# Performance work log

Measured on AMD Instinct MI355X. Metric: run time of the kernel, lower is better.

## Reference

```python
import jax, jax.numpy as jnp
import numpy as np

N_EMBD = 384
N_HEAD = 6
BLOCK_SIZE = 256


def setup_inputs() -> dict:
    key = jax.random.key(0)
    ks = jax.random.split(key, 5)
    B, T = 128, 256
    x = jax.random.normal(ks[0], (B, T, N_EMBD), dtype=jnp.float32)
    # torch nn.Linear weights are (out_features, in_features)
    w_attn = jax.random.normal(ks[1], (3 * N_EMBD, N_EMBD), dtype=jnp.float32) * (1.0 / np.sqrt(N_EMBD))
    b_attn = jax.random.normal(ks[2], (3 * N_EMBD,), dtype=jnp.float32) * 0.02
    w_proj = jax.random.normal(ks[3], (N_EMBD, N_EMBD), dtype=jnp.float32) * (1.0 / np.sqrt(N_EMBD))
    b_proj = jax.random.normal(ks[4], (N_EMBD,), dtype=jnp.float32) * 0.02
    return {"x": x, "w_attn": w_attn, "b_attn": b_attn, "w_proj": w_proj, "b_proj": b_proj}


def reference(x, w_attn, b_attn, w_proj, b_proj):
    B, T, C = x.shape
    hd = C // N_HEAD  # head dim = 64
    qkv = x @ w_attn.T + b_attn                      # [B,T,3C]
    q, k, v = jnp.split(qkv, 3, axis=2)
    # [B,T,C] -> [B,H,T,hd]
    q = q.reshape(B, T, N_HEAD, hd).transpose(0, 2, 1, 3)
    k = k.reshape(B, T, N_HEAD, hd).transpose(0, 2, 1, 3)
    v = v.reshape(B, T, N_HEAD, hd).transpose(0, 2, 1, 3)
    att = jnp.einsum("bhqd,bhkd->bhqk", q, k) * (1.0 / np.sqrt(hd))
    causal = jnp.tril(jnp.ones((T, T), dtype=bool))
    att = jnp.where(causal, att, -jnp.inf)
    att = jax.nn.softmax(att, axis=-1)
    y = jnp.einsum("bhqk,bhkd->bhqd", att, v)        # [B,H,T,hd]
    y = y.transpose(0, 2, 1, 3).reshape(B, T, C)
    return y @ w_proj.T + b_proj
```

## Files before the change

kernel.cpp:

```cpp
#include <hip/hip_runtime.h>
#include <stdint.h>


typedef unsigned short u16;
typedef __attribute__((ext_vector_type(8))) short short8;
typedef __attribute__((ext_vector_type(4))) short short4v;
typedef __attribute__((ext_vector_type(4))) float float4v;

__device__ __forceinline__ u16 f2b(float f){
  union { float f; uint32_t u; } cv; cv.f = f;
  uint32_t u = cv.u;
  u += 0x7FFFu + ((u >> 16) & 1u);
  return (u16)(u >> 16);
}

__device__ __forceinline__ float4v mfma16(short8 a, short8 b, float4v c){
  return __builtin_amdgcn_mfma_f32_16x16x32_bf16(a, b, c, 0, 0, 0);
}

__device__ __forceinline__ void gld16(const void* g, void* l){
  __builtin_amdgcn_global_load_lds((__attribute__((address_space(1))) const void*)g,
                                   (__attribute__((address_space(3))) void*)l, 16, 0, 0);
}

__global__ __launch_bounds__(256) void cvt3(
    const float* __restrict__ a, u16* __restrict__ da, int na,
    const float* __restrict__ b, u16* __restrict__ db, int nb,
    const float* __restrict__ c, u16* __restrict__ dc, int nc)
{
  const int total = na + nb + nc;
  for (int i = blockIdx.x * blockDim.x + threadIdx.x; i < total;
       i += gridDim.x * blockDim.x){
    const float* s; u16* d; int j = i;
    if (j < na)           { s = a; d = da; }
    else if (j < na + nb) { j -= na; s = b; d = db; }
    else                  { j -= na + nb; s = c; d = dc; }
    const float4 v = ((const float4*)s)[j];
    ushort4 o;
    o.x = f2b(v.x); o.y = f2b(v.y); o.z = f2b(v.z); o.w = f2b(v.w);
    ((ushort4*)d)[j] = o;
  }
}

template<bool OUT_BF16>
__global__ __launch_bounds__(256, 2) void gemm_k(
    const u16* __restrict__ A, const u16* __restrict__ B,
    const float* __restrict__ bias, void* __restrict__ Cout,
    const int M, const int N, const int K)
{
  __shared__ u16 Alds[3][256*32];
  __shared__ u16 Blds[3][128*32];
  const int tid  = threadIdx.x;
  const int lane = tid & 63;
  const int wave = tid >> 6;
  const int lrow = lane & 15;
  const int g    = lane >> 4;

  const int NYT   = N >> 7;
  const int id    = blockIdx.x;
  const int local = id >> 3;
  const int xtl   = local / NYT;
  const int yt    = local - xtl * NYT;
  const int xt    = (id & 7) * 16 + xtl;
  const int tm = xt * 256;
  const int tn = yt * 128;
  const int wm = wave * 64;

  float4v acc[4][8];
  #pragma unroll
  for (int i = 0; i < 4; ++i)
    #pragma unroll
    for (int j = 0; j < 8; ++j) acc[i][j] = (float4v){0.f, 0.f, 0.f, 0.f};

  const int srow = lane >> 2;
  const int sg   = ((lane & 3) ^ ((lane >> 3) & 3)) << 3;
  const int key  = (lrow >> 1) & 3;

  auto STAGE = [&](int kt, int buf){
    #pragma unroll
    for (int j = 0; j < 4; ++j){
      const int c = wave * 4 + j;
      const int row = c * 16 + srow;
      gld16(A + (size_t)(tm + row) * K + kt * 32 + sg, &Alds[buf][c * 512]);
    }
    #pragma unroll
    for (int j = 0; j < 2; ++j){
      const int c = wave * 2 + j;
      const int row = c * 16 + srow;
      gld16(B + (size_t)(tn + row) * K + kt * 32 + sg, &Blds[buf][c * 512]);
    }
  };

  const int nkt = K >> 5;
  STAGE(0, 0);
  STAGE(1, 1);
  int b0 = 0;
  for (int kt = 0; kt < nkt; ++kt){
    if (kt + 1 < nkt) asm volatile("s_waitcnt vmcnt(6)" ::: "memory");
    else              asm volatile("s_waitcnt vmcnt(0)" ::: "memory");
    __builtin_amdgcn_s_barrier();

    short8 af[4], bf[8];
    #pragma unroll
    for (int i = 0; i < 4; ++i)
      af[i] = *(const short8*)&Alds[b0][(wm + i * 16 + lrow) * 32 + ((g ^ key) << 3)];
    #pragma unroll
    for (int ni = 0; ni < 8; ++ni)
      bf[ni] = *(const short8*)&Blds[b0][(ni * 16 + lrow) * 32 + ((g ^ key) << 3)];

    asm volatile("s_waitcnt lgkmcnt(0)" ::: "memory");
    __builtin_amdgcn_sched_barrier(0);
    __builtin_amdgcn_s_barrier();

    const int bs = (b0 == 0) ? 2 : b0 - 1;
    if (kt + 2 < nkt) STAGE(kt + 2, bs);

    __builtin_amdgcn_s_setprio(1);
    #pragma unroll
    for (int ni = 0; ni < 8; ++ni)
      #pragma unroll
      for (int mi = 0; mi < 4; ++mi)
        acc[mi][ni] = mfma16(af[mi], bf[ni], acc[mi][ni]);
    __builtin_amdgcn_s_setprio(0);

    b0 = (b0 == 2) ? 0 : b0 + 1;
  }

  #pragma unroll
  for (int mi = 0; mi < 4; ++mi){
    #pragma unroll
    for (int ni = 0; ni < 8; ++ni){
      const int gcol = tn + ni * 16 + lrow;
      const float bs = bias[gcol];
      #pragma unroll
      for (int r = 0; r < 4; ++r){
        const int grow = tm + wm + mi * 16 + g * 4 + r;
        const float v = acc[mi][ni][r] + bs;
        if (OUT_BF16) ((u16*)Cout)[(size_t)grow * N + gcol] = f2b(v);
        else          ((float*)Cout)[(size_t)grow * N + gcol] = v;
      }
    }
  }
}

__global__ __launch_bounds__(256) void attn_k(
    const u16* __restrict__ qkv, u16* __restrict__ y)
{
  __shared__ u16 Klds[256 * 64];
  __shared__ u16 Vt[64 * 256];
  const int tid  = threadIdx.x;
  const int lane = tid & 63;
  const int wave = tid >> 6;
  const int lrow = lane & 15;
  const int g    = lane >> 4;
  const int bh = blockIdx.x;
  const int b = bh / 6, h = bh % 6;
  const u16* qb = qkv + (size_t)b * 256 * 1152 + h * 64;
  const u16* kb = qb + 384;
  const u16* vb = qb + 768;

  #pragma unroll
  for (int j = 0; j < 8; ++j){
    const int c = wave * 8 + j;
    const int row = c * 8 + (lane >> 3);
    const int col = (((lane & 7) ^ (lane >> 3)) << 3);
    gld16(kb + (size_t)row * 1152 + col, &Klds[c * 512]);
  }
  {
    const int d  = lane;
    const int t0 = wave * 64;
    const int sv = d & 15;
    #pragma unroll
    for (int c4 = 0; c4 < 16; ++c4){
      const size_t base = (size_t)(t0 + c4 * 4) * 1152 + d;
      const u16 e0 = vb[base];
      const u16 e1 = vb[base + 1152];
      const u16 e2 = vb[base + 2304];
      const u16 e3 = vb[base + 3456];
      short4v g4; g4[0] = (short)e0; g4[1] = (short)e1; g4[2] = (short)e2; g4[3] = (short)e3;
      const int pos = (t0 >> 2) + (c4 ^ sv);
      *(short4v*)&Vt[(size_t)d * 256 + (pos << 2)] = g4;
    }
  }
  __syncthreads();

  for (int it = 0; it < 4; ++it){
    const int rb = wave + it * 4;
    const int q0 = rb * 16;
    const u16* qrow = qb + (size_t)(q0 + lrow) * 1152 + g * 8;
    const short8 qf0 = *(const short8*)(qrow);
    const short8 qf1 = *(const short8*)(qrow + 32);

    float4v s[16];
    #pragma unroll
    for (int nt = 0; nt < 16; ++nt){
      if (nt <= rb){
        const int row = nt * 16 + lrow;
        const int swk = lrow & 7;
        const short8 k0 = *(const short8*)&Klds[row * 64 + ((g ^ swk) << 3)];
        const short8 k1 = *(const short8*)&Klds[row * 64 + (((4 + g) ^ swk) << 3)];
        float4v a = (float4v){0.f, 0.f, 0.f, 0.f};
        a = mfma16(k0, qf0, a);
        a = mfma16(k1, qf1, a);
        if (nt == rb){
          #pragma unroll
          for (int r = 0; r < 4; ++r)
            a[r] = (g * 4 + r > lrow) ? -1e30f : a[r];
        }
        s[nt] = a;
      }
    }

    float mx = -1e30f;
    #pragma unroll
    for (int nt = 0; nt < 16; ++nt) if (nt <= rb){
      #pragma unroll
      for (int r = 0; r < 4; ++r) mx = fmaxf(mx, s[nt][r]);
    }
    mx = fmaxf(mx, __shfl_xor(mx, 16));
    mx = fmaxf(mx, __shfl_xor(mx, 32));
    float sum = 0.f;
    #pragma unroll
    for (int nt = 0; nt < 16; ++nt) if (nt <= rb){
      #pragma unroll
      for (int r = 0; r < 4; ++r){
        const float p = exp2f((s[nt][r] - mx) * 0.18033688011112042f);
        s[nt][r] = p;
        sum += p;
      }
    }
    sum += __shfl_xor(sum, 16);
    sum += __shfl_xor(sum, 32);
    const float rs = 1.f / sum;
    #pragma unroll
    for (int nt = 0; nt < 16; ++nt) if (nt <= rb) s[nt] *= rs;

    float4v o0 = (float4v){0,0,0,0}, o1 = (float4v){0,0,0,0};
    float4v o2 = (float4v){0,0,0,0}, o3 = (float4v){0,0,0,0};
    const int svr = lrow;
    #pragma unroll
    for (int kt = 0; kt < 8; ++kt){
      if (2 * kt <= rb){
        short8 pa;
        #pragma unroll
        for (int r = 0; r < 4; ++r) pa[r] = (short)f2b(s[2 * kt][r]);
        if (2 * kt + 1 <= rb){
          #pragma unroll
          for (int r = 0; r < 4; ++r) pa[4 + r] = (short)f2b(s[2 * kt + 1][r]);
        } else {
          #pragma unroll
          for (int r = 0; r < 4; ++r) pa[4 + r] = 0;
        }
        const int plo = ((kt * 8 + g) ^ svr) << 2;
        const int phi = ((kt * 8 + 4 + g) ^ svr) << 2;
        #pragma unroll
        for (int dt = 0; dt < 4; ++dt){
          const u16* vrow = &Vt[(size_t)(dt * 16 + lrow) * 256];
          const short4v vlo = *(const short4v*)&vrow[plo];
          const short4v vhi = *(const short4v*)&vrow[phi];
          const short8 bf = __builtin_shufflevector(vlo, vhi, 0,1,2,3,4,5,6,7);
          if      (dt == 0) o0 = mfma16(pa, bf, o0);
          else if (dt == 1) o1 = mfma16(pa, bf, o1);
          else if (dt == 2) o2 = mfma16(pa, bf, o2);
          else              o3 = mfma16(pa, bf, o3);
        }
      }
    }

    u16* yb = y + (size_t)(b * 256 + q0) * 384 + h * 64;
    #pragma unroll
    for (int r = 0; r < 4; ++r){
      const int q = g * 4 + r;
      yb[(size_t)q * 384 +  0 + lrow] = f2b(o0[r]);
      yb[(size_t)q * 384 + 16 + lrow] = f2b(o1[r]);
      yb[(size_t)q * 384 + 32 + lrow] = f2b(o2[r]);
      yb[(size_t)q * 384 + 48 + lrow] = f2b(o3[r]);
    }
  }
}

extern "C" void kernel_launch(void* const* d_in, const int* in_sizes, int n_in,
                              void* d_out, int out_size, void* d_ws, size_t ws_size,
                              hipStream_t stream)
{
  const float* x      = (const float*)d_in[0];
  const float* w_attn = (const float*)d_in[1];
  const float* b_attn = (const float*)d_in[2];
  const float* w_proj = (const float*)d_in[3];
  const float* b_proj = (const float*)d_in[4];
  float* out = (float*)d_out;

  char* ws = (char*)d_ws;
  u16* xb  = (u16*)(ws);
  u16* wab = (u16*)(ws + 25165824);
  u16* wpb = (u16*)(ws + 26050560);
  u16* qkv = (u16*)(ws + 26345472);
  u16* yb  = (u16*)(ws + 101842944);
  if (ws_size < 127008768) return;

  cvt3<<<2048, 256, 0, stream>>>(x, xb, 3145728,
                                 w_attn, wab, 110592,
                                 w_proj, wpb, 36864);
  gemm_k<true ><<<1152, 256, 0, stream>>>(xb, wab, b_attn, qkv, 32768, 1152, 384);
  attn_k<<<768, 256, 0, stream>>>(qkv, yb);
  gemm_k<false><<<384, 256, 0, stream>>>(yb, wpb, b_proj, out, 32768, 384, 384);
}
```

Measured before the change: 122.7 us.

## Write V transposed from QKV GEMM epilogue and restructure GEMM main loop

The QKV GEMM epilogue now writes the V slice directly into a per-head transposed layout [B,H,64,256] in a separate buffer, and Q/K are stored with a narrower row stride of 768. The attention kernel then loads V^T into LDS with async global_load_lds and a new XOR swizzle, instead of doing scalar strided loads and an in-register transpose. Separately, the GEMM k-loop now issues the next stage prefetch before the LDS reads, drops the second barrier and lgkmcnt wait, and removes the setprio calls. The transposed V stores in the epilogue are scattered 2-byte writes, which may cost more than the attention-side transpose they replace. Issuing the prefetch earlier changes the pipelining behaviour of the GEMM.

Measured after the change: 129.1 us. 1.05x slower.

```diff
diff --git a/kernel.cpp b/kernel.cpp
--- a/kernel.cpp
+++ b/kernel.cpp
@@ -42,11 +42,11 @@
   }
 }
 
-template<bool OUT_BF16>
+template<int EPI>
 __global__ __launch_bounds__(256, 2) void gemm_k(
     const u16* __restrict__ A, const u16* __restrict__ B,
     const float* __restrict__ bias, void* __restrict__ Cout,
-    const int M, const int N, const int K)
+    u16* __restrict__ Vt, const int M, const int N, const int K, const int CS)
 {
   __shared__ u16 Alds[3][256*32];
   __shared__ u16 Blds[3][128*32];
@@ -99,6 +99,10 @@
     if (kt + 1 < nkt) asm volatile("s_waitcnt vmcnt(6)" ::: "memory");
     else              asm volatile("s_waitcnt vmcnt(0)" ::: "memory");
     __builtin_amdgcn_s_barrier();
+    __builtin_amdgcn_sched_barrier(0);
+
+    const int bs = (b0 == 0) ? 2 : b0 - 1;
+    if (kt + 2 < nkt) STAGE(kt + 2, bs);
 
     short8 af[4], bf[8];
     #pragma unroll
@@ -107,47 +111,58 @@
     #pragma unroll
     for (int ni = 0; ni < 8; ++ni)
       bf[ni] = *(const short8*)&Blds[b0][(ni * 16 + lrow) * 32 + ((g ^ key) << 3)];
-
-    asm volatile("s_waitcnt lgkmcnt(0)" ::: "memory");
-    __builtin_amdgcn_sched_barrier(0);
-    __builtin_amdgcn_s_barrier();
-
-    const int bs = (b0 == 0) ? 2 : b0 - 1;
-    if (kt + 2 < nkt) STAGE(kt + 2, bs);
-
-    __builtin_amdgcn_s_setprio(1);
     #pragma unroll
     for (int ni = 0; ni < 8; ++ni)
       #pragma unroll
       for (int mi = 0; mi < 4; ++mi)
         acc[mi][ni] = mfma16(af[mi], bf[ni], acc[mi][ni]);
-    __builtin_amdgcn_s_setprio(0);
 
     b0 = (b0 == 2) ? 0 : b0 + 1;
   }
 
-  #pragma unroll
-  for (int mi = 0; mi < 4; ++mi){
+  if (EPI == 1 && tn >= 768){
+    const int bb = tm >> 8;
     #pragma unroll
     for (int ni = 0; ni < 8; ++ni){
-      const int gcol = tn + ni * 16 + lrow;
-      const float bs = bias[gcol];
-      #pragma unroll
-      for (int r = 0; r < 4; ++r){
-        const int grow = tm + wm + mi * 16 + g * 4 + r;
-        const float v = acc[mi][ni][r] + bs;
-        if (OUT_BF16) ((u16*)Cout)[(size_t)grow * N + gcol] = f2b(v);
-        else          ((float*)Cout)[(size_t)grow * N + gcol] = v;
+      const int vcol0 = tn - 768 + ni * 16;
+      const int hh = vcol0 >> 6;
+      const int dd = (vcol0 & 63) + lrow;
+      const float bs = bias[tn + ni * 16 + lrow];
+      u16* vbase = Vt + ((size_t)(bb * 6 + hh) * 64 + dd) * 256;
+      #pragma unroll
+      for (int mi = 0; mi < 4; ++mi){
+        #pragma unroll
+        for (int r = 0; r < 4; ++r){
+          const int t = wm + mi * 16 + g * 4 + r;
+          vbase[t] = f2b(acc[mi][ni][r] + bs);
+        }
+      }
+    }
+  } else {
+    #pragma unroll
+    for (int mi = 0; mi < 4; ++mi){
+      #pragma unroll
+      for (int ni = 0; ni < 8; ++ni){
+        const int gcol = tn + ni * 16 + lrow;
+        const float bs = bias[gcol];
+        #pragma unroll
+        for (int r = 0; r < 4; ++r){
+          const int grow = tm + wm + mi * 16 + g * 4 + r;
+          const float v = acc[mi][ni][r] + bs;
+          if (EPI == 1) ((u16*)Cout)[(size_t)grow * CS + gcol] = f2b(v);
+          else          ((float*)Cout)[(size_t)grow * CS + gcol] = v;
+        }
       }
     }
   }
 }
 
 __global__ __launch_bounds__(256) void attn_k(
-    const u16* __restrict__ qkv, u16* __restrict__ y)
+    const u16* __restrict__ qkv, const u16* __restrict__ vt,
+    u16* __restrict__ y)
 {
   __shared__ u16 Klds[256 * 64];
-  __shared__ u16 Vt[64 * 256];
+  __shared__ u16 Vlds[64 * 256];
   const int tid  = threadIdx.x;
   const int lane = tid & 63;
   const int wave = tid >> 6;
@@ -155,39 +170,30 @@
   const int g    = lane >> 4;
   const int bh = blockIdx.x;
   const int b = bh / 6, h = bh % 6;
-  const u16* qb = qkv + (size_t)b * 256 * 1152 + h * 64;
-  const u16* kb = qb + 384;
-  const u16* vb = qb + 768;
+  const u16* qb  = qkv + (size_t)b * 256 * 768 + h * 64;
+  const u16* kb  = qb + 384;
+  const u16* vtb = vt + (size_t)(b * 6 + h) * 64 * 256;
 
   #pragma unroll
   for (int j = 0; j < 8; ++j){
     const int c = wave * 8 + j;
     const int row = c * 8 + (lane >> 3);
     const int col = (((lane & 7) ^ (lane >> 3)) << 3);
-    gld16(kb + (size_t)row * 1152 + col, &Klds[c * 512]);
-  }
-  {
-    const int d  = lane;
-    const int t0 = wave * 64;
-    const int sv = d & 15;
-    #pragma unroll
-    for (int c4 = 0; c4 < 16; ++c4){
-      const size_t base = (size_t)(t0 + c4 * 4) * 1152 + d;
-      const u16 e0 = vb[base];
-      const u16 e1 = vb[base + 1152];
-      const u16 e2 = vb[base + 2304];
-      const u16 e3 = vb[base + 3456];
-      short4v g4; g4[0] = (short)e0; g4[1] = (short)e1; g4[2] = (short)e2; g4[3] = (short)e3;
-      const int pos = (t0 >> 2) + (c4 ^ sv);
-      *(short4v*)&Vt[(size_t)d * 256 + (pos << 2)] = g4;
-    }
+    gld16(kb + (size_t)row * 768 + col, &Klds[c * 512]);
+  }
+  #pragma unroll
+  for (int j = 0; j < 8; ++j){
+    const int c  = wave * 8 + j;
+    const int dd = c * 2 + (lane >> 5);
+    const int q  = lane & 31;
+    gld16(vtb + (size_t)dd * 256 + ((q ^ (dd & 7)) << 3), &Vlds[c * 512]);
   }
   __syncthreads();
 
   for (int it = 0; it < 4; ++it){
     const int rb = wave + it * 4;
     const int q0 = rb * 16;
-    const u16* qrow = qb + (size_t)(q0 + lrow) * 1152 + g * 8;
+    const u16* qrow = qb + (size_t)(q0 + lrow) * 768 + g * 8;
     const short8 qf0 = *(const short8*)(qrow);
     const short8 qf1 = *(const short8*)(qrow + 32);
 
@@ -237,7 +243,7 @@
 
     float4v o0 = (float4v){0,0,0,0}, o1 = (float4v){0,0,0,0};
     float4v o2 = (float4v){0,0,0,0}, o3 = (float4v){0,0,0,0};
-    const int svr = lrow;
+    const int swk = lrow & 7;
     #pragma unroll
     for (int kt = 0; kt < 8; ++kt){
       if (2 * kt <= rb){
@@ -251,13 +257,13 @@
           #pragma unroll
           for (int r = 0; r < 4; ++r) pa[4 + r] = 0;
         }
-        const int plo = ((kt * 8 + g) ^ svr) << 2;
-        const int phi = ((kt * 8 + 4 + g) ^ svr) << 2;
+        const int plo_e = (((kt * 4 +     (g >> 1)) ^ swk) << 3) + ((g & 1) << 2);
+        const int phi_e = (((kt * 4 + 2 + (g >> 1)) ^ swk) << 3) + ((g & 1) << 2);
         #pragma unroll
         for (int dt = 0; dt < 4; ++dt){
-          const u16* vrow = &Vt[(size_t)(dt * 16 + lrow) * 256];
-          const short4v vlo = *(const short4v*)&vrow[plo];
-          const short4v vhi = *(const short4v*)&vrow[phi];
+          const u16* vrow = &Vlds[(size_t)(dt * 16 + lrow) * 256];
+          const short4v vlo = *(const short4v*)&vrow[plo_e];
+          const short4v vhi = *(const short4v*)&vrow[phi_e];
           const short8 bf = __builtin_shufflevector(vlo, vhi, 0,1,2,3,4,5,6,7);
           if      (dt == 0) o0 = mfma16(pa, bf, o0);
           else if (dt == 1) o1 = mfma16(pa, bf, o1);
@@ -295,13 +301,14 @@
   u16* wab = (u16*)(ws + 25165824);
   u16* wpb = (u16*)(ws + 26050560);
   u16* qkv = (u16*)(ws + 26345472);
+  u16* vt  = (u16*)(ws + 76677120);
   u16* yb  = (u16*)(ws + 101842944);
   if (ws_size < 127008768) return;
 
   cvt3<<<2048, 256, 0, stream>>>(x, xb, 3145728,
                                  w_attn, wab, 110592,
                                  w_proj, wpb, 36864);
-  gemm_k<true ><<<1152, 256, 0, stream>>>(xb, wab, b_attn, qkv, 32768, 1152, 384);
-  attn_k<<<768, 256, 0, stream>>>(qkv, yb);
-  gemm_k<false><<<384, 256, 0, stream>>>(yb, wpb, b_proj, out, 32768, 384, 384);
-}
+  gemm_k<1><<<1152, 256, 0, stream>>>(xb, wab, b_attn, qkv, vt, 32768, 1152, 384, 768);
+  attn_k<<<768, 256, 0, stream>>>(qkv, vt, yb);
+  gemm_k<0><<<384, 256, 0, stream>>>(yb, wpb, b_proj, out, nullptr, 32768, 384, 384, 384);
+}
```
